# Performance work log

Hardware: AMD Instinct MI355X
Metric: run time of the kernel (lower is better)

Reference implementation:

```python
import jax, jax.numpy as jnp
import numpy as np

B, N, D = 8, 256, 64  # batch, n_entities, feature dim


def setup_inputs() -> dict:
    key = jax.random.key(0)
    ks = jax.random.split(key, 8)
    s = 0.02
    return {
        "emb1": jax.random.normal(ks[0], (B, N, D), jnp.float32),
        "emb2": jax.random.normal(ks[1], (B, N, N, D), jnp.float32),
        "W1a": jax.random.normal(ks[2], (3 * D, 128), jnp.float32) * s,
        "b1a": jnp.zeros((128,), jnp.float32),
        "W1b": jax.random.normal(ks[3], (128, D), jnp.float32) * s,
        "b1b": jnp.zeros((D,), jnp.float32),
        "W2a": jax.random.normal(ks[4], (4 * D, 256), jnp.float32) * s,
        "b2a": jnp.zeros((256,), jnp.float32),
        "W2b": jax.random.normal(ks[5], (256, D), jnp.float32) * s,
        "b2b": jnp.zeros((D,), jnp.float32),
    }


def _mlp(x, Wa, ba, Wb, bb):
    h = jax.nn.relu(jnp.einsum("...i,io->...o", x, Wa) + ba)
    return jnp.einsum("...i,io->...o", h, Wb) + bb


def reference(emb1, emb2, W1a, b1a, W1b, b1b, W2a, b2a, W2b, b2b):
    # arity 1: reduce arity-2 embedding over second entity dim (max & min), concat
    red_max = jnp.max(emb2, axis=-2)           # [B,N,D]
    red_min = jnp.min(emb2, axis=-2)           # [B,N,D]
    cat1 = jnp.concatenate([emb1, red_max, red_min], axis=-1)  # [B,N,3D]

    # arity 2: expand arity-1 embedding along a new entity dim, concat with emb2
    exp = jnp.broadcast_to(emb1[:, :, None, :], emb2.shape)    # [B,N,N,D]
    cat2 = jnp.concatenate([exp, emb2], axis=-1)               # [B,N,N,2D]

    # permutation gather: position (i,j) gets [cat2[j,i], cat2[i,j]] along features
    perm2 = jnp.concatenate([jnp.transpose(cat2, (0, 2, 1, 3)), cat2], axis=-1)  # [B,N,N,4D]

    out1 = _mlp(cat1, W1a, b1a, W1b, b1b)    # [B,N,D]
    out2 = _mlp(perm2, W2a, b2a, W2b, b2b)   # [B,N,N,D]
    return (out1, out2)
```

## Files before the change

### kernel.cpp

```cpp
#include <hip/hip_runtime.h>
#include <hip/hip_bf16.h>

typedef __bf16 bf16x8 __attribute__((ext_vector_type(8)));
typedef float f32x4 __attribute__((ext_vector_type(4)));
typedef unsigned int u32;
typedef unsigned short u16;
typedef u32 u32x4 __attribute__((ext_vector_type(4)));
typedef u16 u16x4 __attribute__((ext_vector_type(4)));
typedef u16 u16x8 __attribute__((ext_vector_type(8)));

__device__ __forceinline__ u16 f2bf(float x) {
  u32 u = __float_as_uint(x);
  return (u16)((u + 0x7FFFu + ((u >> 16) & 1u)) >> 16);
}
__device__ __forceinline__ u16 cvt_bf16(float x) {
  __bf16 h = (__bf16)x;
  return __builtin_bit_cast(u16, h);
}
__device__ __forceinline__ float bf2f(u16 h) {
  return __uint_as_float((u32)h << 16);
}

__device__ __forceinline__ bf16x8 ld_frag_lds(const u16* base, int byteOff) {
  u32x4 v = *(const u32x4*)((const char*)base + byteOff);
  return __builtin_bit_cast(bf16x8, v);
}
__device__ __forceinline__ bf16x8 ld_frag_glb(const u16* p) {
  u32x4 v = *(const u32x4*)p;
  return __builtin_bit_cast(bf16x8, v);
}

__global__ void prep_w_kernel(const float* __restrict__ W2a, const float* __restrict__ W2b,
                              u16* __restrict__ wfA, u16* __restrict__ wfB2) {
  int t = blockIdx.x * 256 + threadIdx.x;
  if (t < 8192) {
    int lane = t & 63;
    int ks = (t >> 6) & 7;
    int ntg = t >> 9;
    int col = (ntg << 4) + (lane & 15);
    int kb = (ks << 5) + ((lane >> 4) << 3);
#pragma unroll
    for (int q = 0; q < 8; ++q)
      wfA[t * 8 + q] = f2bf(W2a[(kb + q) * 256 + col]);
  } else if (t < 10240) {
    int t2i = t - 8192;
    int lane = t2i & 63;
    int dt = (t2i >> 6) & 3;
    int tt = (t2i >> 8) & 1;
    int w = t2i >> 9;
    int g = lane >> 4, c = lane & 15;
    int col = (dt << 4) + c;
#pragma unroll
    for (int q = 0; q < 8; ++q) {
      int pi = (q < 4) ? (g * 4 + q) : (16 + g * 4 + (q - 4));
      int n = w * 64 + tt * 32 + pi;
      wfB2[t2i * 8 + q] = f2bf(W2b[n * 64 + col]);
    }
  }
}

__global__ __launch_bounds__(256) void out1_kernel(
    const float* __restrict__ emb1, const float* __restrict__ emb2,
    const float* __restrict__ W1a, const float* __restrict__ b1a,
    const float* __restrict__ W1b, const float* __restrict__ b1b,
    float* __restrict__ out1) {
  int bi = blockIdx.x;
  int t = threadIdx.x;
  __shared__ float smax[4][64];
  __shared__ float smin[4][64];
  __shared__ float cat1[192];
  __shared__ float h[128];

  int d = t & 63, q = t >> 6;
  const float* base = emb2 + (size_t)bi * 256 * 64;
  float vmax = -INFINITY, vmin = INFINITY;
  for (int j = q; j < 256; j += 4) {
    float v = base[j * 64 + d];
    vmax = fmaxf(vmax, v);
    vmin = fminf(vmin, v);
  }
  smax[q][d] = vmax;
  smin[q][d] = vmin;
  __syncthreads();
  if (t < 64) {
    float mx = fmaxf(fmaxf(smax[0][t], smax[1][t]), fmaxf(smax[2][t], smax[3][t]));
    float mn = fminf(fminf(smin[0][t], smin[1][t]), fminf(smin[2][t], smin[3][t]));
    cat1[t] = emb1[bi * 64 + t];
    cat1[64 + t] = mx;
    cat1[128 + t] = mn;
  }
  __syncthreads();
  if (t < 128) {
    float acc = b1a[t];
    for (int k = 0; k < 192; ++k) acc += cat1[k] * W1a[k * 128 + t];
    h[t] = fmaxf(acc, 0.f);
  }
  __syncthreads();
  if (t < 64) {
    float acc = b1b[t];
    for (int k = 0; k < 128; ++k) acc += h[k] * W1b[k * 64 + t];
    out1[bi * 64 + t] = acc;
  }
}

__global__ __launch_bounds__(256, 2) void out2_kernel(
    const float* __restrict__ emb1, const float* __restrict__ emb2,
    const float* __restrict__ b2a, const float* __restrict__ b2b,
    const u16* __restrict__ wfA, const u16* __restrict__ wfB2,
    float* __restrict__ out2) {
  __shared__ __align__(16) u16 SH[16384];

  int blk = blockIdx.x;
  int b = blk >> 10;
  int i = (blk >> 2) & 255;
  int j0 = (blk & 3) << 6;
  int t = threadIdx.x;
  int lane = t & 63;
  int w = t >> 6;
  int lr = lane & 15;
  int lg = lane >> 4;

  {
    int r = t >> 2;
    int c16 = (t & 3) << 4;
    const float* s0 = emb1 + ((b << 8) + j0 + r) * 64;
    const float* s1 = emb2 + ((((size_t)(b << 8) + j0 + r) << 8) + i) * 64;
    const float* s2 = emb1 + ((b << 8) + i) * 64;
    const float* s3 = emb2 + ((((size_t)(b << 8) + i) << 8) + (j0 + r)) * 64;
    const float* srcs[4] = {s0, s1, s2, s3};
#pragma unroll
    for (int seg = 0; seg < 4; ++seg) {
      const float* src = srcs[seg];
#pragma unroll
      for (int u = 0; u < 2; ++u) {
        int d = c16 + (u << 3);
        float4 v0 = *(const float4*)(src + d);
        float4 v1 = *(const float4*)(src + d + 4);
        u16x8 o = {cvt_bf16(v0.x), cvt_bf16(v0.y), cvt_bf16(v0.z), cvt_bf16(v0.w),
                   cvt_bf16(v1.x), cvt_bf16(v1.y), cvt_bf16(v1.z), cvt_bf16(v1.w)};
        int byteOff = (r * 512 + ((seg << 6) + d) * 2) ^ ((r & 7) << 4);
        *(u16x8*)((char*)SH + byteOff) = o;
      }
    }
  }
  __syncthreads();

  f32x4 acc1[4][4];
#pragma unroll
  for (int m = 0; m < 4; ++m)
#pragma unroll
    for (int nt = 0; nt < 4; ++nt) acc1[m][nt] = (f32x4){0.f, 0.f, 0.f, 0.f};

#pragma unroll
  for (int ks = 0; ks < 8; ++ks) {
    int kByte = (ks << 6) + (lg << 4);
    bf16x8 a[4];
#pragma unroll
    for (int m = 0; m < 4; ++m) {
      int row = (m << 4) + lr;
      a[m] = ld_frag_lds(SH, (row * 512 + kByte) ^ ((lr & 7) << 4));
    }
    bf16x8 bw[4];
#pragma unroll
    for (int nt = 0; nt < 4; ++nt)
      bw[nt] = ld_frag_glb(wfA + (size_t)((((w << 2) + nt) * 8 + ks) * 64 + lane) * 8);
#pragma unroll
    for (int m = 0; m < 4; ++m)
#pragma unroll
      for (int nt = 0; nt < 4; ++nt)
        acc1[m][nt] = __builtin_amdgcn_mfma_f32_16x16x32_bf16(bw[nt], a[m], acc1[m][nt], 0, 0, 0);
  }

  __syncthreads();

  f32x4 acc2[4][4];
#pragma unroll
  for (int m = 0; m < 4; ++m)
#pragma unroll
    for (int dt = 0; dt < 4; ++dt) acc2[m][dt] = (f32x4){0.f, 0.f, 0.f, 0.f};

#pragma unroll
  for (int t2 = 0; t2 < 2; ++t2) {
    int nbase = (w << 6) + (t2 << 5) + (lg << 2);
    float4 ba = *(const float4*)(b2a + nbase);
    float4 bb = *(const float4*)(b2a + nbase + 16);
    bf16x8 h[4];
#pragma unroll
    for (int m = 0; m < 4; ++m) {
      f32x4 pa = acc1[m][2 * t2];
      f32x4 pb = acc1[m][2 * t2 + 1];
      u16x8 hp = {cvt_bf16(fmaxf(pa[0] + ba.x, 0.f)), cvt_bf16(fmaxf(pa[1] + ba.y, 0.f)),
                  cvt_bf16(fmaxf(pa[2] + ba.z, 0.f)), cvt_bf16(fmaxf(pa[3] + ba.w, 0.f)),
                  cvt_bf16(fmaxf(pb[0] + bb.x, 0.f)), cvt_bf16(fmaxf(pb[1] + bb.y, 0.f)),
                  cvt_bf16(fmaxf(pb[2] + bb.z, 0.f)), cvt_bf16(fmaxf(pb[3] + bb.w, 0.f))};
      h[m] = __builtin_bit_cast(bf16x8, hp);
    }
#pragma unroll
    for (int dt = 0; dt < 4; ++dt) {
      bf16x8 wf = ld_frag_glb(wfB2 + (size_t)(((((w << 1) + t2) << 2) + dt) * 64 + lane) * 8);
#pragma unroll
      for (int m = 0; m < 4; ++m)
        acc2[m][dt] = __builtin_amdgcn_mfma_f32_16x16x32_bf16(wf, h[m], acc2[m][dt], 0, 0, 0);
    }
  }

  char* red = (char*)SH;
#pragma unroll
  for (int dt = 0; dt < 4; ++dt) {
    if (dt != w) {
      int s = dt - (dt > w ? 1 : 0);
#pragma unroll
      for (int m = 0; m < 4; ++m) {
        f32x4 p = acc2[m][dt];
        u16x4 o = {cvt_bf16(p[0]), cvt_bf16(p[1]), cvt_bf16(p[2]), cvt_bf16(p[3])};
        *(u16x4*)(red + (((w * 12 + s * 4 + m) << 9) + (lane << 3))) = o;
      }
    }
  }
  __syncthreads();

  f32x4 accO[4];
#pragma unroll
  for (int m = 0; m < 4; ++m) {
    accO[m] = acc2[m][0];
#pragma unroll
    for (int dt = 1; dt < 4; ++dt)
      if (w == dt) accO[m] = acc2[m][dt];
  }
#pragma unroll
  for (int wp = 0; wp < 4; ++wp) {
    if (wp != w) {
      int s = w - (w > wp ? 1 : 0);
#pragma unroll
      for (int m = 0; m < 4; ++m) {
        u16x4 o = *(const u16x4*)(red + (((wp * 12 + s * 4 + m) << 9) + (lane << 3)));
        accO[m][0] += bf2f(o[0]);
        accO[m][1] += bf2f(o[1]);
        accO[m][2] += bf2f(o[2]);
        accO[m][3] += bf2f(o[3]);
      }
    }
  }

  float4 bias2 = *(const float4*)(b2b + (w << 4) + (lg << 2));
  float* obase = out2 + (((size_t)(b << 8) + i) * 256 + j0) * 64 + (w << 4) + (lg << 2);
#pragma unroll
  for (int m = 0; m < 4; ++m) {
    float4 v = {accO[m][0] + bias2.x, accO[m][1] + bias2.y,
                accO[m][2] + bias2.z, accO[m][3] + bias2.w};
    *(float4*)(obase + (size_t)((m << 4) + lr) * 64) = v;
  }
}

extern "C" void kernel_launch(void* const* d_in, const int* in_sizes, int n_in,
                              void* d_out, int out_size, void* d_ws, size_t ws_size,
                              hipStream_t stream) {
  const float* emb1 = (const float*)d_in[0];
  const float* emb2 = (const float*)d_in[1];
  const float* W1a  = (const float*)d_in[2];
  const float* b1a  = (const float*)d_in[3];
  const float* W1b  = (const float*)d_in[4];
  const float* b1b  = (const float*)d_in[5];
  const float* W2a  = (const float*)d_in[6];
  const float* b2a  = (const float*)d_in[7];
  const float* W2b  = (const float*)d_in[8];
  const float* b2b  = (const float*)d_in[9];

  float* out = (float*)d_out;
  u16* wfA  = (u16*)d_ws;
  u16* wfB2 = wfA + 65536;

  prep_w_kernel<<<40, 256, 0, stream>>>(W2a, W2b, wfA, wfB2);
  out1_kernel<<<2048, 256, 0, stream>>>(emb1, emb2, W1a, b1a, W1b, b1b, out);
  out2_kernel<<<8192, 256, 0, stream>>>(emb1, emb2, b2a, b2b, wfA, wfB2,
                                        out + 8 * 256 * 64);
}
```

Before: 159.5 us.

## Double out2 tile to 128 rows per block with 8 waves

Each out2 block now processes 128 j rows instead of 64, using 512 threads split into two M-halves that share the same weight fragments and bias loads. Grid size halves and LDS usage doubles, with the cross-wave reduction buffer partitioned per M-half. The intent is to amortize per-block overhead and weight fetches; the 512x2 launch bound tightens the register budget and may cause spills or lower occupancy.

```diff
diff --git a/kernel.cpp b/kernel.cpp
--- a/kernel.cpp
+++ b/kernel.cpp
@@ -103,30 +103,33 @@
   }
 }
 
-__global__ __launch_bounds__(256, 2) void out2_kernel(
+__global__ __launch_bounds__(512, 2) void out2_kernel(
     const float* __restrict__ emb1, const float* __restrict__ emb2,
     const float* __restrict__ b2a, const float* __restrict__ b2b,
     const u16* __restrict__ wfA, const u16* __restrict__ wfB2,
     float* __restrict__ out2) {
-  __shared__ __align__(16) u16 SH[16384];
+  __shared__ __align__(16) u16 SH[32768];
 
   int blk = blockIdx.x;
-  int b = blk >> 10;
-  int i = (blk >> 2) & 255;
-  int j0 = (blk & 3) << 6;
+  int b = blk >> 9;
+  int i = (blk >> 1) & 255;
+  int j0 = (blk & 1) << 7;
   int t = threadIdx.x;
   int lane = t & 63;
-  int w = t >> 6;
+  int w8 = t >> 6;
+  int mw = w8 >> 2;
+  int nw = w8 & 3;
   int lr = lane & 15;
   int lg = lane >> 4;
 
   {
     int r = t >> 2;
     int c16 = (t & 3) << 4;
-    const float* s0 = emb1 + ((b << 8) + j0 + r) * 64;
-    const float* s1 = emb2 + ((((size_t)(b << 8) + j0 + r) << 8) + i) * 64;
+    int j = j0 + r;
+    const float* s0 = emb1 + ((b << 8) + j) * 64;
+    const float* s1 = emb2 + ((((size_t)(b << 8) + j) << 8) + i) * 64;
     const float* s2 = emb1 + ((b << 8) + i) * 64;
-    const float* s3 = emb2 + ((((size_t)(b << 8) + i) << 8) + (j0 + r)) * 64;
+    const float* s3 = emb2 + ((((size_t)(b << 8) + i) << 8) + j) * 64;
     const float* srcs[4] = {s0, s1, s2, s3};
 #pragma unroll
     for (int seg = 0; seg < 4; ++seg) {
@@ -157,13 +160,13 @@
     bf16x8 a[4];
 #pragma unroll
     for (int m = 0; m < 4; ++m) {
-      int row = (m << 4) + lr;
+      int row = (mw << 6) + (m << 4) + lr;
       a[m] = ld_frag_lds(SH, (row * 512 + kByte) ^ ((lr & 7) << 4));
     }
     bf16x8 bw[4];
 #pragma unroll
     for (int nt = 0; nt < 4; ++nt)
-      bw[nt] = ld_frag_glb(wfA + (size_t)((((w << 2) + nt) * 8 + ks) * 64 + lane) * 8);
+      bw[nt] = ld_frag_glb(wfA + (size_t)((((nw << 2) + nt) * 8 + ks) * 64 + lane) * 8);
 #pragma unroll
     for (int m = 0; m < 4; ++m)
 #pragma unroll
@@ -181,7 +184,7 @@
 
 #pragma unroll
   for (int t2 = 0; t2 < 2; ++t2) {
-    int nbase = (w << 6) + (t2 << 5) + (lg << 2);
+    int nbase = (nw << 6) + (t2 << 5) + (lg << 2);
     float4 ba = *(const float4*)(b2a + nbase);
     float4 bb = *(const float4*)(b2a + nbase + 16);
     bf16x8 h[4];
@@ -197,23 +200,23 @@
     }
 #pragma unroll
     for (int dt = 0; dt < 4; ++dt) {
-      bf16x8 wf = ld_frag_glb(wfB2 + (size_t)(((((w << 1) + t2) << 2) + dt) * 64 + lane) * 8);
+      bf16x8 wf = ld_frag_glb(wfB2 + (size_t)(((((nw << 1) + t2) << 2) + dt) * 64 + lane) * 8);
 #pragma unroll
       for (int m = 0; m < 4; ++m)
         acc2[m][dt] = __builtin_amdgcn_mfma_f32_16x16x32_bf16(wf, h[m], acc2[m][dt], 0, 0, 0);
     }
   }
 
-  char* red = (char*)SH;
+  char* red = (char*)SH + mw * 24576;
 #pragma unroll
   for (int dt = 0; dt < 4; ++dt) {
-    if (dt != w) {
-      int s = dt - (dt > w ? 1 : 0);
+    if (dt != nw) {
+      int s = dt - (dt > nw ? 1 : 0);
 #pragma unroll
       for (int m = 0; m < 4; ++m) {
         f32x4 p = acc2[m][dt];
         u16x4 o = {cvt_bf16(p[0]), cvt_bf16(p[1]), cvt_bf16(p[2]), cvt_bf16(p[3])};
-        *(u16x4*)(red + (((w * 12 + s * 4 + m) << 9) + (lane << 3))) = o;
+        *(u16x4*)(red + (((nw * 12 + s * 4 + m) << 9) + (lane << 3))) = o;
       }
     }
   }
@@ -225,12 +228,12 @@
     accO[m] = acc2[m][0];
 #pragma unroll
     for (int dt = 1; dt < 4; ++dt)
-      if (w == dt) accO[m] = acc2[m][dt];
+      if (nw == dt) accO[m] = acc2[m][dt];
   }
 #pragma unroll
   for (int wp = 0; wp < 4; ++wp) {
-    if (wp != w) {
-      int s = w - (w > wp ? 1 : 0);
+    if (wp != nw) {
+      int s = nw - (nw > wp ? 1 : 0);
 #pragma unroll
       for (int m = 0; m < 4; ++m) {
         u16x4 o = *(const u16x4*)(red + (((wp * 12 + s * 4 + m) << 9) + (lane << 3)));
@@ -242,8 +245,9 @@
     }
   }
 
-  float4 bias2 = *(const float4*)(b2b + (w << 4) + (lg << 2));
-  float* obase = out2 + (((size_t)(b << 8) + i) * 256 + j0) * 64 + (w << 4) + (lg << 2);
+  float4 bias2 = *(const float4*)(b2b + (nw << 4) + (lg << 2));
+  float* obase = out2 + (((size_t)(b << 8) + i) * 256 + j0 + (mw << 6)) * 64 +
+                 (nw << 4) + (lg << 2);
 #pragma unroll
   for (int m = 0; m < 4; ++m) {
     float4 v = {accO[m][0] + bias2.x, accO[m][1] + bias2.y,
@@ -272,6 +276,6 @@
 
   prep_w_kernel<<<40, 256, 0, stream>>>(W2a, W2b, wfA, wfB2);
   out1_kernel<<<2048, 256, 0, stream>>>(emb1, emb2, W1a, b1a, W1b, b1b, out);
-  out2_kernel<<<8192, 256, 0, stream>>>(emb1, emb2, b2a, b2b, wfA, wfB2,
+  out2_kernel<<<4096, 512, 0, stream>>>(emb1, emb2, b2a, b2b, wfA, wfB2,
                                         out + 8 * 256 * 64);
 }
```

After: 175.2 us. 1.1x slower.

## Load GEMM1 A-fragments directly from global into registers, bypassing LDS staging

Applied to the files above, without the earlier changes.

Removes the LDS staging of the concatenated 4D input tile and its barrier. Each wave now loads its MFMA A-fragments straight from emb1/emb2 in global memory and converts them to bf16 in registers. The strided transposed emb2 reads are issued first to hide their latency, and the shared emb1 row is broadcast across all m tiles. LDS shrinks, which may raise occupancy, but every wave now re-reads the same A data from global/L2 instead of sharing it once through LDS.

```diff
diff --git a/kernel.cpp b/kernel.cpp
--- a/kernel.cpp
+++ b/kernel.cpp
@@ -20,10 +20,10 @@
 __device__ __forceinline__ float bf2f(u16 h) {
   return __uint_as_float((u32)h << 16);
 }
-
-__device__ __forceinline__ bf16x8 ld_frag_lds(const u16* base, int byteOff) {
-  u32x4 v = *(const u32x4*)((const char*)base + byteOff);
-  return __builtin_bit_cast(bf16x8, v);
+__device__ __forceinline__ bf16x8 cvt8(float4 a, float4 b) {
+  u16x8 o = {cvt_bf16(a.x), cvt_bf16(a.y), cvt_bf16(a.z), cvt_bf16(a.w),
+             cvt_bf16(b.x), cvt_bf16(b.y), cvt_bf16(b.z), cvt_bf16(b.w)};
+  return __builtin_bit_cast(bf16x8, o);
 }
 __device__ __forceinline__ bf16x8 ld_frag_glb(const u16* p) {
   u32x4 v = *(const u32x4*)p;
@@ -108,7 +108,7 @@
     const float* __restrict__ b2a, const float* __restrict__ b2b,
     const u16* __restrict__ wfA, const u16* __restrict__ wfB2,
     float* __restrict__ out2) {
-  __shared__ __align__(16) u16 SH[16384];
+  __shared__ __align__(16) u16 SH[12288];
 
   int blk = blockIdx.x;
   int b = blk >> 10;
@@ -120,30 +120,23 @@
   int lr = lane & 15;
   int lg = lane >> 4;
 
+  bf16x8 xs1[4][2];
+#pragma unroll
+  for (int m = 0; m < 4; ++m) {
+    const float* p = emb2 + ((((size_t)(b << 8) + j0 + (m << 4) + lr) << 8) + i) * 64 + (lg << 3);
+#pragma unroll
+    for (int kk = 0; kk < 2; ++kk)
+      xs1[m][kk] = cvt8(*(const float4*)(p + (kk << 5)),
+                        *(const float4*)(p + (kk << 5) + 4));
+  }
+  bf16x8 xs2[2];
   {
-    int r = t >> 2;
-    int c16 = (t & 3) << 4;
-    const float* s0 = emb1 + ((b << 8) + j0 + r) * 64;
-    const float* s1 = emb2 + ((((size_t)(b << 8) + j0 + r) << 8) + i) * 64;
-    const float* s2 = emb1 + ((b << 8) + i) * 64;
-    const float* s3 = emb2 + ((((size_t)(b << 8) + i) << 8) + (j0 + r)) * 64;
-    const float* srcs[4] = {s0, s1, s2, s3};
-#pragma unroll
-    for (int seg = 0; seg < 4; ++seg) {
-      const float* src = srcs[seg];
-#pragma unroll
-      for (int u = 0; u < 2; ++u) {
-        int d = c16 + (u << 3);
-        float4 v0 = *(const float4*)(src + d);
-        float4 v1 = *(const float4*)(src + d + 4);
-        u16x8 o = {cvt_bf16(v0.x), cvt_bf16(v0.y), cvt_bf16(v0.z), cvt_bf16(v0.w),
-                   cvt_bf16(v1.x), cvt_bf16(v1.y), cvt_bf16(v1.z), cvt_bf16(v1.w)};
-        int byteOff = (r * 512 + ((seg << 6) + d) * 2) ^ ((r & 7) << 4);
-        *(u16x8*)((char*)SH + byteOff) = o;
-      }
-    }
-  }
-  __syncthreads();
+    const float* p = emb1 + (((b << 8) + i) << 6) + (lg << 3);
+#pragma unroll
+    for (int kk = 0; kk < 2; ++kk)
+      xs2[kk] = cvt8(*(const float4*)(p + (kk << 5)),
+                     *(const float4*)(p + (kk << 5) + 4));
+  }
 
   f32x4 acc1[4][4];
 #pragma unroll
@@ -151,15 +144,7 @@
 #pragma unroll
     for (int nt = 0; nt < 4; ++nt) acc1[m][nt] = (f32x4){0.f, 0.f, 0.f, 0.f};
 
-#pragma unroll
-  for (int ks = 0; ks < 8; ++ks) {
-    int kByte = (ks << 6) + (lg << 4);
-    bf16x8 a[4];
-#pragma unroll
-    for (int m = 0; m < 4; ++m) {
-      int row = (m << 4) + lr;
-      a[m] = ld_frag_lds(SH, (row * 512 + kByte) ^ ((lr & 7) << 4));
-    }
+  auto g1step = [&](int ks, const bf16x8* a4) {
     bf16x8 bw[4];
 #pragma unroll
     for (int nt = 0; nt < 4; ++nt)
@@ -168,10 +153,40 @@
     for (int m = 0; m < 4; ++m)
 #pragma unroll
       for (int nt = 0; nt < 4; ++nt)
-        acc1[m][nt] = __builtin_amdgcn_mfma_f32_16x16x32_bf16(bw[nt], a[m], acc1[m][nt], 0, 0, 0);
-  }
-
-  __syncthreads();
+        acc1[m][nt] = __builtin_amdgcn_mfma_f32_16x16x32_bf16(bw[nt], a4[m], acc1[m][nt], 0, 0, 0);
+  };
+
+#pragma unroll
+  for (int kk = 0; kk < 2; ++kk) {
+    bf16x8 a4[4];
+#pragma unroll
+    for (int m = 0; m < 4; ++m) {
+      const float* p = emb1 + (((b << 8) + j0 + (m << 4) + lr) << 6) + (lg << 3) + (kk << 5);
+      a4[m] = cvt8(*(const float4*)p, *(const float4*)(p + 4));
+    }
+    g1step(kk, a4);
+  }
+#pragma unroll
+  for (int kk = 0; kk < 2; ++kk) {
+    bf16x8 a4[4];
+#pragma unroll
+    for (int m = 0; m < 4; ++m) {
+      const float* p = emb2 + ((((size_t)(b << 8) + i) << 8) + j0 + (m << 4) + lr) * 64 +
+                       (lg << 3) + (kk << 5);
+      a4[m] = cvt8(*(const float4*)p, *(const float4*)(p + 4));
+    }
+    g1step(6 + kk, a4);
+  }
+#pragma unroll
+  for (int kk = 0; kk < 2; ++kk) {
+    bf16x8 a4[4] = {xs2[kk], xs2[kk], xs2[kk], xs2[kk]};
+    g1step(4 + kk, a4);
+  }
+#pragma unroll
+  for (int kk = 0; kk < 2; ++kk) {
+    bf16x8 a4[4] = {xs1[0][kk], xs1[1][kk], xs1[2][kk], xs1[3][kk]};
+    g1step(2 + kk, a4);
+  }
 
   f32x4 acc2[4][4];
 #pragma unroll
```

After: 276.7 us. +73.5%, slower.
